# Kernel tuning notes

Measured on AMD Instinct MI355X. Metric: run time of the kernel, lower is better.

## Reference

```python
import jax, jax.numpy as jnp
import numpy as np

SIZE = 1024
CODE_DIM = 256

def setup_inputs() -> dict:
    key = jax.random.key(0)
    k1, k2 = jax.random.split(key)
    z = jax.random.normal(k1, (32, CODE_DIM, 32, 32), dtype=jnp.float32)
    # nn.Embedding weight init: uniform(-1/size, 1/size)
    emb_weight = jax.random.uniform(k2, (SIZE, CODE_DIM), dtype=jnp.float32,
                                    minval=-1.0 / SIZE, maxval=1.0 / SIZE)
    return {"z": z, "emb_weight": emb_weight}

def reference(z, emb_weight):
    n, c, h, w = z.shape
    # [n, h, w, c] -> [n*h*w, c]
    z_ = jnp.transpose(z, (0, 2, 3, 1)).reshape(-1, c)
    # squared euclidean distances to all codes: ||z||^2 - 2 z.W^T + ||W||^2
    distances = (jnp.sum(z_ ** 2, axis=1, keepdims=True)
                 - 2.0 * jnp.matmul(z_, emb_weight.T)
                 + jnp.sum(emb_weight ** 2, axis=1)[None, :])
    encoding_indices = jnp.argmin(distances, axis=1).reshape(n, h, w)
    # gather codes and move channel back: [n, h, w, c] -> [n, c, h, w]
    quantized = jnp.transpose(emb_weight[encoding_indices], (0, 3, 1, 2))
    straight_through = jax.lax.stop_gradient(quantized - z) + z
    return (quantized, straight_through, encoding_indices)
```

## Files before the change

kernel.cpp:

```cpp
#include <hip/hip_runtime.h>
#include <cfloat>


#define P_TOTAL   32768
#define N_CODES   1024
#define Q_ELEMS   8388608
#define EPS_SCREEN 4.0e-3f
#define CAND_CAP  64

typedef __attribute__((ext_vector_type(8))) short bf16x8;
typedef __attribute__((ext_vector_type(4))) float f32x4;

#define GLOAD16(gsrc, ldst) \
  __builtin_amdgcn_global_load_lds((const __attribute__((address_space(1))) void*)(gsrc), \
                                   (__attribute__((address_space(3))) void*)(ldst), 16, 0, 0)

__device__ __forceinline__ unsigned short f2bf(float f) {
    unsigned u = __builtin_bit_cast(unsigned, f);
    u += 0x7FFF + ((u >> 16) & 1);
    return (unsigned short)(u >> 16);
}

__device__ __forceinline__ float sq_sep(float v) {
    float t = v * v;
    asm volatile("" : "+v"(t));
    return t;
}

__global__ void k0t_transpose(const float* __restrict__ wemb, float* __restrict__ wt) {
    __shared__ float tile[64 * 65];
    const int tid = threadIdx.x;
    const int ct = blockIdx.x >> 2, kt = blockIdx.x & 3;
    const int c0 = ct * 64, k0 = kt * 64;
    const int rr = tid >> 4, cg = tid & 15;
    #pragma unroll
    for (int i = 0; i < 4; ++i) {
        const int row = i * 16 + rr;
        const float4 v = *(const float4*)&wemb[(size_t)(c0 + row) * 256 + k0 + cg * 4];
        tile[row * 65 + cg * 4 + 0] = v.x;
        tile[row * 65 + cg * 4 + 1] = v.y;
        tile[row * 65 + cg * 4 + 2] = v.z;
        tile[row * 65 + cg * 4 + 3] = v.w;
    }
    __syncthreads();
    #pragma unroll
    for (int i = 0; i < 4; ++i) {
        const int krow = i * 16 + rr;
        float4 v;
        v.x = tile[(cg * 4 + 0) * 65 + krow];
        v.y = tile[(cg * 4 + 1) * 65 + krow];
        v.z = tile[(cg * 4 + 2) * 65 + krow];
        v.w = tile[(cg * 4 + 3) * 65 + krow];
        *(float4*)&wt[(size_t)(k0 + krow) * 1024 + c0 + cg * 4] = v;
    }
}

__global__ void k0w_pack(const float* __restrict__ wemb, unsigned short* __restrict__ whi) {
    const int t = blockIdx.x * 256 + threadIdx.x;
    const int c = t >> 5, g = t & 31;
    const float4 v0 = *(const float4*)&wemb[(size_t)c * 256 + g * 8];
    const float4 v1 = *(const float4*)&wemb[(size_t)c * 256 + g * 8 + 4];
    bf16x8 hv;
    hv[0] = (short)f2bf(v0.x); hv[1] = (short)f2bf(v0.y);
    hv[2] = (short)f2bf(v0.z); hv[3] = (short)f2bf(v0.w);
    hv[4] = (short)f2bf(v1.x); hv[5] = (short)f2bf(v1.y);
    hv[6] = (short)f2bf(v1.z); hv[7] = (short)f2bf(v1.w);
    const int gs = g ^ (c & 7);
    *(bf16x8*)(whi + (size_t)c * 256 + gs * 8) = hv;
}

#define T16S 280
__global__ void k0z_pack(const float* __restrict__ z, unsigned short* __restrict__ zhi) {
    __shared__ unsigned short t16[64 * T16S];
    const int tid = threadIdx.x;
    const int n = blockIdx.x >> 4, hc = blockIdx.x & 15;
    const int hw0 = hc * 64;
    const int w = tid >> 6, hl = tid & 63;
    #pragma unroll
    for (int i = 0; i < 64; ++i) {
        const int k = i * 4 + w;
        const float v = z[((size_t)(n * 256 + k) << 10) + hw0 + hl];
        t16[hl * T16S + k] = f2bf(v);
    }
    __syncthreads();
    const int row = tid >> 2, cp = tid & 3;
    const size_t p0 = (size_t)(n * 1024 + hw0);
    #pragma unroll
    for (int i = 0; i < 8; ++i) {
        const int chunk = i * 4 + cp;
        *(bf16x8*)(zhi + (p0 + row) * 256 + chunk * 8) =
            *(const bf16x8*)&t16[row * T16S + chunk * 8];
    }
}

__global__ void k1_wsq(const float* __restrict__ wemb, float* __restrict__ wsq,
                       int* __restrict__ candCnt) {
    const int b = blockIdx.x, tid = threadIdx.x;
    if (b >= 4) { candCnt[(b - 4) * 256 + tid] = 0; return; }
    const int c = b * 256 + tid;
    const float* base = wemb + (size_t)c * 256;
    float half[2];
    #pragma unroll
    for (int h = 0; h < 2; ++h) {
        const float* x = base + h * 128;
        float r[8];
        #pragma unroll
        for (int j = 0; j < 8; ++j) r[j] = sq_sep(x[j]);
        for (int i = 8; i < 128; i += 8) {
            #pragma unroll
            for (int j = 0; j < 8; ++j) r[j] += sq_sep(x[i + j]);
        }
        half[h] = ((r[0] + r[1]) + (r[2] + r[3])) + ((r[4] + r[5]) + (r[6] + r[7]));
    }
    wsq[c] = half[0] + half[1];
}

__launch_bounds__(256, 4)
__global__ void k2s_screen(const unsigned short* __restrict__ zhi,
                           const unsigned short* __restrict__ whi,
                           const float* __restrict__ wsq,
                           unsigned short* __restrict__ candC,
                           float* __restrict__ candD,
                           int* __restrict__ candCnt) {
    __shared__ unsigned short Bs[2][32 * 256];
    const int tid = threadIdx.x, bid = blockIdx.x;
    const int pgrp = bid >> 1, half = bid & 1;
    const int w = tid >> 6, l = tid & 63;
    const int la = l & 15, kg = l >> 4;
    const int m0 = pgrp * 64 + w * 16;
    const int cb0 = half * 512;

    bf16x8 af[8];
    #pragma unroll
    for (int ks = 0; ks < 8; ++ks)
        af[ks] = *(const bf16x8*)(zhi + (size_t)(m0 + la) * 256 + ks * 32 + kg * 8);

    float rg[4];
    #pragma unroll
    for (int r = 0; r < 4; ++r) rg[r] = FLT_MAX;

#define STAGEB(buf, cb_) do {                                                  \
    const unsigned short* src_ = whi + (size_t)(cb_) * 256;                    \
    _Pragma("unroll")                                                          \
    for (int i_ = 0; i_ < 4; ++i_)                                             \
        GLOAD16(src_ + i_ * 2048 + tid * 8, &Bs[buf][i_ * 2048 + tid * 8]);    \
} while (0)

    STAGEB(0, cb0);
    __syncthreads();

    for (int ch = 0; ch < 16; ++ch) {
        const int cur = ch & 1;
        const int cb = cb0 + ch * 32;
        if (ch < 15) STAGEB(cur ^ 1, cb + 32);

        float wsqv[2];
        #pragma unroll
        for (int nf = 0; nf < 2; ++nf) wsqv[nf] = wsq[cb + nf * 16 + la];

        f32x4 acc[2];
        #pragma unroll
        for (int nf = 0; nf < 2; ++nf) acc[nf] = (f32x4){0.f, 0.f, 0.f, 0.f};

        #pragma unroll
        for (int ks = 0; ks < 8; ++ks) {
            bf16x8 bfv[2];
            #pragma unroll
            for (int nf = 0; nf < 2; ++nf) {
                const int cl = nf * 16 + la;
                const int slot = (ks * 4 + kg) ^ (cl & 7);
                bfv[nf] = *(const bf16x8*)&Bs[cur][cl * 256 + slot * 8];
            }
            #pragma unroll
            for (int nf = 0; nf < 2; ++nf)
                acc[nf] = __builtin_amdgcn_mfma_f32_16x16x32_bf16(
                    af[ks], bfv[nf], acc[nf], 0, 0, 0);
        }

        float da[2][4];
        #pragma unroll
        for (int nf = 0; nf < 2; ++nf)
            #pragma unroll
            for (int r = 0; r < 4; ++r)
                da[nf][r] = __builtin_fmaf(-2.f, acc[nf][r], wsqv[nf]);

        #pragma unroll
        for (int r = 0; r < 4; ++r) {
            float mv = fminf(da[0][r], da[1][r]);
            #pragma unroll
            for (int off = 1; off < 16; off <<= 1)
                mv = fminf(mv, __shfl_xor(mv, off));
            rg[r] = fminf(rg[r], mv);
        }

        #pragma unroll
        for (int nf = 0; nf < 2; ++nf)
            #pragma unroll
            for (int r = 0; r < 4; ++r)
                if (da[nf][r] <= rg[r] + EPS_SCREEN) {
                    const int p = pgrp * 64 + w * 16 + kg * 4 + r;
                    const int slot = atomicAdd(&candCnt[p], 1);
                    if (slot < CAND_CAP) {
                        candC[(size_t)p * CAND_CAP + slot] =
                            (unsigned short)(cb + nf * 16 + la);
                        candD[(size_t)p * CAND_CAP + slot] = da[nf][r];
                    }
                }

        __syncthreads();
    }
#undef STAGEB
}

__launch_bounds__(256, 4)
__global__ void k2r_rescore(const float* __restrict__ z, const float* __restrict__ wemb,
                            const float* __restrict__ wsq,
                            const unsigned short* __restrict__ candC,
                            const float* __restrict__ candD,
                            const int* __restrict__ candCnt,
                            float* __restrict__ idx_out) {
    __shared__ float t32[32 * 256];
    const int tid = threadIdx.x;
    const int wv = tid >> 6, l = tid & 63;
    const int p0 = blockIdx.x * 32;
    const int n = p0 >> 10, hw0 = p0 & 1023;

    const int pl = tid >> 3, slot = tid & 7;
    const int p = p0 + pl;
    const int count = candCnt[p];
    const int c0raw = candC[(size_t)p * CAND_CAP + slot];
    const float da0 = candD[(size_t)p * CAND_CAP + slot];

    const int row = l & 31;
    const int xmr = (row & 7) * 4;
    #pragma unroll
    for (int i = 0; i < 8; ++i) {
        const int k4 = i * 32 + wv * 8 + (l >> 5) * 4;
        const size_t zb = ((size_t)(n * 256 + k4) << 10) + hw0 + row;
        float4 v;
        v.x = z[zb];
        v.y = z[zb + 1024];
        v.z = z[zb + 2048];
        v.w = z[zb + 3072];
        *(float4*)&t32[row * 256 + (k4 ^ xmr)] = v;
    }

    bool need;
    float thr = 0.f;
    if (count <= CAND_CAP) {
        const int nr = (count + 7) >> 3;
        float m = (slot < count) ? da0 : FLT_MAX;
        for (int rr = 1; rr < nr; ++rr) {
            const int s = rr * 8 + slot;
            if (s < count) m = fminf(m, candD[(size_t)p * CAND_CAP + s]);
        }
        #pragma unroll
        for (int off = 1; off < 8; off <<= 1) m = fminf(m, __shfl_xor(m, off));
        thr = m + EPS_SCREEN;

        int V;
        int soleC = N_CODES;
        {
            const bool v0 = (slot < count) && (da0 <= thr);
            const unsigned long long mask = __ballot(v0);
            V = __popcll((mask >> ((l >> 3) * 8)) & 0xFFull);
            if (v0) soleC = c0raw;
        }
        for (int rr = 1; rr < nr; ++rr) {
            const int s = rr * 8 + slot;
            bool vs = false;
            if (s < count) {
                vs = (candD[(size_t)p * CAND_CAP + s] <= thr);
                if (vs && soleC == N_CODES) soleC = candC[(size_t)p * CAND_CAP + s];
            }
            const unsigned long long mask = __ballot(vs);
            V += __popcll((mask >> ((l >> 3) * 8)) & 0xFFull);
        }
        if (V == 1 && soleC != N_CODES) idx_out[p] = (float)soleC;
        need = (V >= 2);
    } else {
        need = true;
    }

    __syncthreads();

    if (!need) return;

    const float* zrow = &t32[pl * 256];
    const int xm = (pl & 7) * 4;

    float halfv[2];
    #pragma unroll
    for (int h = 0; h < 2; ++h) {
        float r[8];
        {
            const f32x4 a = *(const f32x4*)&zrow[(h * 128) ^ xm];
            const f32x4 b = *(const f32x4*)&zrow[(h * 128 + 4) ^ xm];
            #pragma unroll
            for (int j = 0; j < 4; ++j) { r[j] = sq_sep(a[j]); r[4 + j] = sq_sep(b[j]); }
        }
        for (int i = 8; i < 128; i += 8) {
            const f32x4 a = *(const f32x4*)&zrow[(h * 128 + i) ^ xm];
            const f32x4 b = *(const f32x4*)&zrow[(h * 128 + i + 4) ^ xm];
            #pragma unroll
            for (int j = 0; j < 4; ++j) { r[j] += sq_sep(a[j]); r[4 + j] += sq_sep(b[j]); }
        }
        halfv[h] = ((r[0] + r[1]) + (r[2] + r[3])) + ((r[4] + r[5]) + (r[6] + r[7]));
    }
    const float zsv = halfv[0] + halfv[1];

#define DOT_CHAIN(wb_, dot_) do {                                              \
    _Pragma("unroll")                                                          \
    for (int kb = 0; kb < 256; kb += 8) {                                      \
        const f32x4 za = *(const f32x4*)&zrow[kb ^ xm];                        \
        const f32x4 zb4 = *(const f32x4*)&zrow[(kb + 4) ^ xm];                 \
        const float4 wa = *(const float4*)&(wb_)[kb];                          \
        const float4 wc = *(const float4*)&(wb_)[kb + 4];                      \
        dot_ = __builtin_fmaf(za[0], wa.x, dot_);                              \
        dot_ = __builtin_fmaf(za[1], wa.y, dot_);                              \
        dot_ = __builtin_fmaf(za[2], wa.z, dot_);                              \
        dot_ = __builtin_fmaf(za[3], wa.w, dot_);                              \
        dot_ = __builtin_fmaf(zb4[0], wc.x, dot_);                             \
        dot_ = __builtin_fmaf(zb4[1], wc.y, dot_);                             \
        dot_ = __builtin_fmaf(zb4[2], wc.z, dot_);                             \
        dot_ = __builtin_fmaf(zb4[3], wc.w, dot_);                             \
    }                                                                          \
} while (0)

    float bd = FLT_MAX;
    int bc = N_CODES;

    if (count <= CAND_CAP) {
        const int nr = (count + 7) >> 3;
        for (int rr = 0; rr < nr; ++rr) {
            const int s = rr * 8 + slot;
            int c; float das;
            if (rr == 0) { c = c0raw; das = da0; }
            else if (s < count) {
                c = candC[(size_t)p * CAND_CAP + s];
                das = candD[(size_t)p * CAND_CAP + s];
            } else { c = N_CODES; das = FLT_MAX; }
            if (s < count && das <= thr) {
                const float* wb = wemb + (size_t)c * 256;
                float dot = 0.f;
                DOT_CHAIN(wb, dot);
                const float d = __builtin_fmaf(-2.f, dot, zsv) + wsq[c];
                if (d < bd || (d == bd && c < bc)) { bd = d; bc = c; }
            }
        }
    } else {
        for (int rr = 0; rr < 128; ++rr) {
            const int c = rr * 8 + slot;
            const float* wb = wemb + (size_t)c * 256;
            float dot = 0.f;
            DOT_CHAIN(wb, dot);
            const float d = __builtin_fmaf(-2.f, dot, zsv) + wsq[c];
            if (d < bd || (d == bd && c < bc)) { bd = d; bc = c; }
        }
    }
#undef DOT_CHAIN

    #pragma unroll
    for (int off = 1; off < 8; off <<= 1) {
        const float od = __shfl_xor(bd, off);
        const int   oi = __shfl_xor(bc, off);
        if (od < bd || (od == bd && oi < bc)) { bd = od; bc = oi; }
    }
    if (slot == 0) idx_out[p] = (float)bc;
}

__global__ void k3_gather(const float* __restrict__ z, const float* __restrict__ wtf,
                          const float* __restrict__ idxf,
                          float* __restrict__ out0, float* __restrict__ out1) {
    __shared__ float wcol[1024];
    const int tid = threadIdx.x;
    const int b = blockIdx.x;
    const int c = b & 255, n = b >> 8;
    *(float4*)&wcol[tid * 4] = *(const float4*)&wtf[(size_t)c * 1024 + tid * 4];
    __syncthreads();

    const size_t zo = (((size_t)(n * 256 + c)) << 10) + tid * 4;
    const float4 zv = *(const float4*)&z[zo];
    const float4 iv = *(const float4*)&idxf[n * 1024 + tid * 4];
    float4 qv, st;
    qv.x = wcol[(int)iv.x]; st.x = (qv.x - zv.x) + zv.x;
    qv.y = wcol[(int)iv.y]; st.y = (qv.y - zv.y) + zv.y;
    qv.z = wcol[(int)iv.z]; st.z = (qv.z - zv.z) + zv.z;
    qv.w = wcol[(int)iv.w]; st.w = (qv.w - zv.w) + zv.w;
    *(float4*)&out0[zo] = qv;
    *(float4*)&out1[zo] = st;
}

extern "C" void kernel_launch(void* const* d_in, const int* in_sizes, int n_in,
                              void* d_out, int out_size, void* d_ws, size_t ws_size,
                              hipStream_t stream) {
    const float* z = (const float*)d_in[0];
    const float* wemb = (const float*)d_in[1];
    float* out = (float*)d_out;
    float* out0 = out;
    float* out1 = out + Q_ELEMS;
    float* oidx = out + 2 * Q_ELEMS;
    unsigned short* zhi = (unsigned short*)out0;
    unsigned short* candC = (unsigned short*)(out0 + 4194304);
    float* candD = out0 + 5242880;
    int* candCnt = (int*)(out0 + 7340032);
    unsigned short* whi = (unsigned short*)out1;
    float* wsq = (float*)d_ws;
    float* wtf = (float*)d_ws + 1024;

    k0t_transpose<<<64, 256, 0, stream>>>(wemb, wtf);
    k0w_pack<<<128, 256, 0, stream>>>(wemb, whi);
    k0z_pack<<<512, 256, 0, stream>>>(z, zhi);
    k1_wsq<<<132, 256, 0, stream>>>(wemb, wsq, candCnt);
    k2s_screen<<<1024, 256, 0, stream>>>(zhi, whi, wsq, candC, candD, candCnt);
    k2r_rescore<<<P_TOTAL / 32, 256, 0, stream>>>(z, wemb, wsq, candC, candD, candCnt, oidx);
    k3_gather<<<8192, 256, 0, stream>>>(z, wtf, oidx, out0, out1);
}
```

Baseline: 167.0 us.

## Double rows per wave in screening kernel, split codebook into quarters

Each wave now holds two 16-row A fragments, so every B fragment read from LDS feeds two MFMAs. Each block covers 128 points against a quarter of the codebook (8 chunks) instead of 64 points against half. The block index is remapped so that blocks sharing a point group are spread across the grid. The aim is to halve LDS B traffic per MFMA. In exchange, register pressure rises, and with fewer codes seen per block the running minimum is looser, which may admit more candidates through the atomics.

```diff
diff --git a/kernel.cpp b/kernel.cpp
--- a/kernel.cpp
+++ b/kernel.cpp
@@ -124,20 +124,26 @@
                            int* __restrict__ candCnt) {
     __shared__ unsigned short Bs[2][32 * 256];
     const int tid = threadIdx.x, bid = blockIdx.x;
-    const int pgrp = bid >> 1, half = bid & 1;
+    const int pgrp = (bid & 7) | ((bid >> 5) << 3);
+    const int q = (bid >> 3) & 3;
     const int w = tid >> 6, l = tid & 63;
     const int la = l & 15, kg = l >> 4;
-    const int m0 = pgrp * 64 + w * 16;
-    const int cb0 = half * 512;
-
-    bf16x8 af[8];
-    #pragma unroll
-    for (int ks = 0; ks < 8; ++ks)
-        af[ks] = *(const bf16x8*)(zhi + (size_t)(m0 + la) * 256 + ks * 32 + kg * 8);
-
-    float rg[4];
-    #pragma unroll
-    for (int r = 0; r < 4; ++r) rg[r] = FLT_MAX;
+    const int m0 = pgrp * 128 + w * 32;
+    const int cb0 = q * 256;
+
+    bf16x8 af[2][8];
+    #pragma unroll
+    for (int mi = 0; mi < 2; ++mi)
+        #pragma unroll
+        for (int ks = 0; ks < 8; ++ks)
+            af[mi][ks] = *(const bf16x8*)(zhi + (size_t)(m0 + mi * 16 + la) * 256
+                                          + ks * 32 + kg * 8);
+
+    float rg[2][4];
+    #pragma unroll
+    for (int mi = 0; mi < 2; ++mi)
+        #pragma unroll
+        for (int r = 0; r < 4; ++r) rg[mi][r] = FLT_MAX;
 
 #define STAGEB(buf, cb_) do {                                                  \
     const unsigned short* src_ = whi + (size_t)(cb_) * 256;                    \
@@ -149,63 +155,70 @@
     STAGEB(0, cb0);
     __syncthreads();
 
-    for (int ch = 0; ch < 16; ++ch) {
+    for (int ch = 0; ch < 8; ++ch) {
         const int cur = ch & 1;
         const int cb = cb0 + ch * 32;
-        if (ch < 15) STAGEB(cur ^ 1, cb + 32);
+        if (ch < 7) STAGEB(cur ^ 1, cb + 32);
 
         float wsqv[2];
         #pragma unroll
         for (int nf = 0; nf < 2; ++nf) wsqv[nf] = wsq[cb + nf * 16 + la];
 
-        f32x4 acc[2];
-        #pragma unroll
-        for (int nf = 0; nf < 2; ++nf) acc[nf] = (f32x4){0.f, 0.f, 0.f, 0.f};
+        f32x4 acc[2][2];
+        #pragma unroll
+        for (int mi = 0; mi < 2; ++mi)
+            #pragma unroll
+            for (int nf = 0; nf < 2; ++nf) acc[mi][nf] = (f32x4){0.f, 0.f, 0.f, 0.f};
 
         #pragma unroll
         for (int ks = 0; ks < 8; ++ks) {
-            bf16x8 bfv[2];
             #pragma unroll
             for (int nf = 0; nf < 2; ++nf) {
                 const int cl = nf * 16 + la;
                 const int slot = (ks * 4 + kg) ^ (cl & 7);
-                bfv[nf] = *(const bf16x8*)&Bs[cur][cl * 256 + slot * 8];
+                const bf16x8 bf = *(const bf16x8*)&Bs[cur][cl * 256 + slot * 8];
+                acc[0][nf] = __builtin_amdgcn_mfma_f32_16x16x32_bf16(
+                    af[0][ks], bf, acc[0][nf], 0, 0, 0);
+                acc[1][nf] = __builtin_amdgcn_mfma_f32_16x16x32_bf16(
+                    af[1][ks], bf, acc[1][nf], 0, 0, 0);
             }
+        }
+
+        float da[2][2][4];
+        #pragma unroll
+        for (int mi = 0; mi < 2; ++mi)
             #pragma unroll
             for (int nf = 0; nf < 2; ++nf)
-                acc[nf] = __builtin_amdgcn_mfma_f32_16x16x32_bf16(
-                    af[ks], bfv[nf], acc[nf], 0, 0, 0);
-        }
-
-        float da[2][4];
-        #pragma unroll
-        for (int nf = 0; nf < 2; ++nf)
-            #pragma unroll
-            for (int r = 0; r < 4; ++r)
-                da[nf][r] = __builtin_fmaf(-2.f, acc[nf][r], wsqv[nf]);
-
-        #pragma unroll
-        for (int r = 0; r < 4; ++r) {
-            float mv = fminf(da[0][r], da[1][r]);
-            #pragma unroll
-            for (int off = 1; off < 16; off <<= 1)
-                mv = fminf(mv, __shfl_xor(mv, off));
-            rg[r] = fminf(rg[r], mv);
-        }
-
-        #pragma unroll
-        for (int nf = 0; nf < 2; ++nf)
-            #pragma unroll
-            for (int r = 0; r < 4; ++r)
-                if (da[nf][r] <= rg[r] + EPS_SCREEN) {
-                    const int p = pgrp * 64 + w * 16 + kg * 4 + r;
-                    const int slot = atomicAdd(&candCnt[p], 1);
-                    if (slot < CAND_CAP) {
-                        candC[(size_t)p * CAND_CAP + slot] =
-                            (unsigned short)(cb + nf * 16 + la);
-                        candD[(size_t)p * CAND_CAP + slot] = da[nf][r];
+                #pragma unroll
+                for (int r = 0; r < 4; ++r)
+                    da[mi][nf][r] = __builtin_fmaf(-2.f, acc[mi][nf][r], wsqv[nf]);
+
+        #pragma unroll
+        for (int mi = 0; mi < 2; ++mi)
+            #pragma unroll
+            for (int r = 0; r < 4; ++r) {
+                float mv = fminf(da[mi][0][r], da[mi][1][r]);
+                #pragma unroll
+                for (int off = 1; off < 16; off <<= 1)
+                    mv = fminf(mv, __shfl_xor(mv, off));
+                rg[mi][r] = fminf(rg[mi][r], mv);
+            }
+
+        #pragma unroll
+        for (int mi = 0; mi < 2; ++mi)
+            #pragma unroll
+            for (int nf = 0; nf < 2; ++nf)
+                #pragma unroll
+                for (int r = 0; r < 4; ++r)
+                    if (da[mi][nf][r] <= rg[mi][r] + EPS_SCREEN) {
+                        const int p = m0 + mi * 16 + kg * 4 + r;
+                        const int slot = atomicAdd(&candCnt[p], 1);
+                        if (slot < CAND_CAP) {
+                            candC[(size_t)p * CAND_CAP + slot] =
+                                (unsigned short)(cb + nf * 16 + la);
+                            candD[(size_t)p * CAND_CAP + slot] = da[mi][nf][r];
+                        }
                     }
-                }
 
         __syncthreads();
     }
```

Result: slower. 201.1 us (+20.4%).
